# Optimization experiments

Hardware: AMD Instinct MI355X
Metric: run time of the kernel (lower is better)

The kernel has to match this reference:

```python
import math
import jax, jax.numpy as jnp
from jax import lax
import numpy as np

SCORE_THR = 0.5
IOU_THR = 0.7
MIN_SIZE = 1.0
BBOX_CLIP = math.log(1000.0 / 16.0)

FEAT_SIZES = [100, 50, 25, 13, 7]
STRIDES = [8, 16, 32, 64, 128]
RATIOS = (0.5, 1.0, 2.0)
C = 256
A = 3
N = 2


def _make_priors(fs, stride):
    base = stride * 4.0
    ys, xs = np.meshgrid(np.arange(fs), np.arange(fs), indexing='ij')
    cx = (xs + 0.5) * stride
    cy = (ys + 0.5) * stride
    pri = []
    for r in RATIOS:
        w = base / np.sqrt(r)
        h = base * np.sqrt(r)
        pri.append(np.stack([cx - w / 2, cy - h / 2, cx + w / 2, cy + h / 2], axis=-1))
    pri = np.stack(pri, axis=2)  # (fs, fs, A, 4): H,W,A order matches permute/reshape
    return jnp.asarray(pri.reshape(-1, 4), dtype=jnp.float32)


def setup_inputs():
    key = jax.random.key(0)
    ks = jax.random.split(key, 8)
    inp = {}
    for i, fs in enumerate(FEAT_SIZES):
        inp[f'fmap{i}'] = jax.random.normal(jax.random.fold_in(ks[0], i), (N, C, fs, fs), dtype=jnp.float32)
        inp[f'priors{i}'] = _make_priors(fs, STRIDES[i])
    sc = 0.02
    inp['conv_w'] = jax.random.normal(ks[1], (C, C, 3, 3), jnp.float32) * sc
    inp['conv_b'] = jnp.zeros((C,), jnp.float32)
    inp['log_w'] = jax.random.normal(ks[2], (A, C, 1, 1), jnp.float32) * sc
    inp['log_b'] = jnp.zeros((A,), jnp.float32)
    inp['reg_w'] = jax.random.normal(ks[3], (A * 4, C, 1, 1), jnp.float32) * sc
    inp['reg_b'] = jnp.zeros((A * 4,), jnp.float32)
    inp['imsizes'] = jnp.full((N, 2), 800, dtype=jnp.int32)  # (h, w) per image
    inp['lvtop'] = 500
    inp['imtop'] = 100
    return inp


def _conv(x, w, b, pad):
    y = lax.conv_general_dilated(x, w, (1, 1), pad, dimension_numbers=('NCHW', 'OIHW', 'NCHW'))
    return y + b[None, :, None, None]


def _decode(reg, pri):
    pw = pri[..., 2] - pri[..., 0]
    ph = pri[..., 3] - pri[..., 1]
    pcx = pri[..., 0] + 0.5 * pw
    pcy = pri[..., 1] + 0.5 * ph
    dx, dy = reg[..., 0], reg[..., 1]
    dw = jnp.minimum(reg[..., 2], BBOX_CLIP)
    dh = jnp.minimum(reg[..., 3], BBOX_CLIP)
    cx = dx * pw + pcx
    cy = dy * ph + pcy
    w = jnp.exp(dw) * pw
    h = jnp.exp(dh) * ph
    return jnp.stack([cx - 0.5 * w, cy - 0.5 * h, cx + 0.5 * w, cy + 0.5 * h], axis=-1)


def _head(x, priors, conv_w, conv_b, log_w, log_b, reg_w, reg_b, lvtop):
    n = x.shape[0]
    h = jax.nn.relu(_conv(x, conv_w, conv_b, 'SAME'))
    reg = _conv(h, reg_w, reg_b, 'VALID').transpose(0, 2, 3, 1).reshape(n, -1, 4)
    log = _conv(h, log_w, log_b, 'VALID').transpose(0, 2, 3, 1).reshape(n, -1)
    k = min(lvtop, log.shape[1])
    vals, top = lax.top_k(log, k)                           # (n, k)
    reg = jnp.take_along_axis(reg, top[..., None], axis=1)  # (n, k, 4)
    pri = priors[top]                                       # (n, k, 4)
    return _decode(reg, pri), vals, k


def _box_iou(a, b):
    area_a = (a[:, 2] - a[:, 0]) * (a[:, 3] - a[:, 1])
    area_b = (b[:, 2] - b[:, 0]) * (b[:, 3] - b[:, 1])
    lt = jnp.maximum(a[:, None, :2], b[None, :, :2])
    rb = jnp.minimum(a[:, None, 2:], b[None, :, 2:])
    wh = jnp.clip(rb - lt, 0.0)
    inter = wh[..., 0] * wh[..., 1]
    return inter / (area_a[:, None] + area_b[None, :] - inter + 1e-9)


def _forward(fmaps, priors, conv_w, conv_b, log_w, log_b, reg_w, reg_b, imsizes, lvtop, imtop):
    tups = [_head(x, p, conv_w, conv_b, log_w, log_b, reg_w, reg_b, lvtop)
            for x, p in zip(fmaps, priors)]
    boxes = jnp.concatenate([t[0] for t in tups], axis=1)                 # (n, D, 4)
    obj = jax.nn.sigmoid(jnp.concatenate([t[1] for t in tups], axis=1))   # (n, D)
    lvlen = jnp.asarray([t[2] for t in tups])
    n, D = obj.shape
    boxes = boxes.reshape(-1, 4)
    obj = obj.reshape(-1)
    K = n * D
    imidx = jnp.arange(K) // D
    valid = obj >= SCORE_THR                                # score filter (masked, not nonzero)
    hw = imsizes[imidx].astype(jnp.float32)                 # (K, 2) = (h, w)
    x1 = jnp.clip(boxes[:, 0], 0.0, hw[:, 1])
    y1 = jnp.clip(boxes[:, 1], 0.0, hw[:, 0])
    x2 = jnp.clip(boxes[:, 2], 0.0, hw[:, 1])
    y2 = jnp.clip(boxes[:, 3], 0.0, hw[:, 0])
    boxes = jnp.stack([x1, y1, x2, y2], axis=-1)
    valid &= (x2 - x1 >= MIN_SIZE) & (y2 - y1 >= MIN_SIZE)  # remove_small
    lvidx = jnp.searchsorted(jnp.cumsum(lvlen), jnp.arange(K) % D, side='right')
    groups = imidx * 10 + lvidx
    scores = jnp.where(valid, obj, -jnp.inf)
    order = jnp.argsort(-scores)                            # global score order; groups gate suppression
    b, g, v, ii = boxes[order], groups[order], valid[order], imidx[order]
    iou = _box_iou(b, b)                                    # (K, K)
    ar = jnp.arange(K)
    def body(i, keep):
        sup = (iou[i] > IOU_THR) & (g == g[i]) & (ar > i)
        return jnp.where(keep[i], keep & ~sup, keep)
    keep = lax.fori_loop(0, K, body, v)                     # greedy batched NMS
    def select(i):
        m = keep & (ii == i)
        sel = jnp.argsort(~m)[:imtop]                       # stable: kept boxes in score order
        val = m[sel]
        bx = jnp.where(val[:, None], b[sel], 0.0)
        ix = jnp.where(val, i, -1)
        return bx, ix
    bx, ix = jax.vmap(select)(jnp.arange(n))
    return bx.reshape(n * imtop, 4), ix.reshape(n * imtop)


def reference(fmap0, fmap1, fmap2, fmap3, fmap4, priors0, priors1, priors2, priors3, priors4,
              conv_w, conv_b, log_w, log_b, reg_w, reg_b, imsizes, lvtop, imtop):
    return _forward([fmap0, fmap1, fmap2, fmap3, fmap4],
                    [priors0, priors1, priors2, priors3, priors4],
                    conv_w, conv_b, log_w, log_b, reg_w, reg_b, imsizes, lvtop, imtop)
```

## Files before the change

kernel.cpp:

```cpp
#include <hip/hip_runtime.h>
#include <math.h>


#define N_IMG 2
#define C_CH  256
#define D_PER 2147
#define K_TOT 4294
#define CONV_BLOCKS 1912
#define CPX 239

typedef double v4d __attribute__((ext_vector_type(4)));

__constant__ int c_Ml[5]     = {30000, 7500, 1875, 507, 147};
__constant__ int c_kl[5]     = {500, 500, 500, 500, 147};
__constant__ int c_logoff[5] = {0, 60000, 75000, 78750, 79764};
__constant__ int c_regoff[5] = {0, 240000, 300000, 315000, 319056};
__constant__ int c_fs[5]     = {100, 50, 25, 13, 7};
__constant__ int c_npt[5]    = {13, 7, 4, 2, 1};
__constant__ int c_E[5]      = {10000, 2500, 625, 169, 49};
__constant__ int c_cumbl[6]  = {0, 1352, 1744, 1872, 1904, 1912};
__constant__ int c_hcum[6]   = {0, 157, 197, 207, 210, 211};
__constant__ size_t c_hoff[5] = {0, 5120000, 6400000, 6720000, 6806528};

template <typename T>
__global__ __launch_bounds__(256) void conv_fused_kernel(
    const float* __restrict__ x0, const float* __restrict__ x1,
    const float* __restrict__ x2, const float* __restrict__ x3,
    const float* __restrict__ x4, const float* __restrict__ wraw,
    const float* __restrict__ bias, T* __restrict__ h) {
  __shared__ __align__(16) double s_in[2][960];
  int tid = threadIdx.x;
  int bid = (blockIdx.x & 7) * CPX + (blockIdx.x >> 3);
  int l = 0;
  while (bid >= c_cumbl[l + 1]) ++l;
  int r = bid - c_cumbl[l];
  int fs = c_fs[l], npt = c_npt[l];
  int tiles = npt * npt;
  int tile = r % tiles;
  int cn = r / tiles;
  int cobi = cn & 3, n = cn >> 2;
  int ptx = tile % npt, pty = tile / npt;
  int px0 = ptx * 8, py0 = pty * 8;
  int E = fs * fs;
  const float* xl;
  switch (l) {
    case 0: xl = x0; break;
    case 1: xl = x1; break;
    case 2: xl = x2; break;
    case 3: xl = x3; break;
    default: xl = x4; break;
  }
  const float* xn = xl + (size_t)n * C_CH * E;
  T* hl = h + c_hoff[l];

  int lane = tid & 63;
  int wv = tid >> 6;
  int lx = lane & 15;
  int lk = lane >> 4;

  double ind0 = (lk == 0) ? 1.0 : 0.0;
  v4d pr1 = __builtin_amdgcn_mfma_f64_16x16x4f64((double)lx, ind0,
                                                 (v4d)0.0, 0, 0, 0);
  v4d pr2 = __builtin_amdgcn_mfma_f64_16x16x4f64(ind0, (double)lx,
                                                 (v4d)0.0, 0, 0, 0);
  int coL[4], pxL[4];
#pragma unroll
  for (int q = 0; q < 4; ++q) {
    coL[q] = (int)pr1[q];
    pxL[q] = (int)pr2[q];
  }

  int in_dst[4], in_src[4];
#pragma unroll
  for (int it = 0; it < 4; ++it) {
    int idx = tid + it * 256;
    in_dst[it] = -1;
    in_src[it] = -1;
    if (idx < 800) {
      int ci = idx / 100, rr2 = idx % 100;
      int hy = rr2 / 10, hx = rr2 % 10;
      int gy = py0 - 1 + hy, gx = px0 - 1 + hx;
      in_dst[it] = ci * 120 + hy * 12 + hx;
      if (gy >= 0 && gy < fs && gx >= 0 && gx < fs)
        in_src[it] = ci * E + gy * fs + gx;
    }
  }

  int bOff[4];
#pragma unroll
  for (int p = 0; p < 4; ++p) {
    int pxidx = p * 16 + lx;
    bOff[p] = lk * 120 + (pxidx >> 3) * 12 + (pxidx & 7);
  }

  v4d acc[4];
#pragma unroll
  for (int p = 0; p < 4; ++p) acc[p] = (v4d)0.0;

  const float* wp0 =
      wraw + (size_t)(cobi * 64 + wv * 16 + lx) * 2304;

  float wcur[18], wnxt[18];
  {
    const float* a = wp0 + lk * 9;
    const float* b = wp0 + (4 + lk) * 9;
#pragma unroll
    for (int t = 0; t < 9; ++t) {
      wcur[t] = a[t];
      wcur[9 + t] = b[t];
    }
  }
  {
    float v0[4];
#pragma unroll
    for (int it = 0; it < 4; ++it)
      v0[it] = (in_dst[it] >= 0 && in_src[it] >= 0) ? xn[in_src[it]] : 0.f;
#pragma unroll
    for (int it = 0; it < 4; ++it)
      if (in_dst[it] >= 0) s_in[0][in_dst[it]] = (double)v0[it];
  }
  __syncthreads();

  for (int it = 0; it < 32; ++it) {
    int buf = it & 1;
    bool more = (it + 1 < 32);
    float inx[4];
    if (more) {
      const float* xc1 = xn + (size_t)(it + 1) * 8 * E;
#pragma unroll
      for (int s = 0; s < 4; ++s)
        inx[s] = (in_dst[s] >= 0 && in_src[s] >= 0) ? xc1[in_src[s]] : 0.f;
      const float* a = wp0 + ((it + 1) * 8 + lk) * 9;
      const float* b = wp0 + ((it + 1) * 8 + 4 + lk) * 9;
#pragma unroll
      for (int t = 0; t < 9; ++t) {
        wnxt[t] = a[t];
        wnxt[9 + t] = b[t];
      }
    }
    const double* bbA = s_in[buf];
    const double* bbB = s_in[buf] + 480;
#pragma unroll
    for (int ky = 0; ky < 3; ++ky) {
#pragma unroll
      for (int kx = 0; kx < 3; ++kx) {
        int tap = ky * 3 + kx;
        int boff = ky * 12 + kx;
        double avA = (double)wcur[tap];
#pragma unroll
        for (int p = 0; p < 4; ++p) {
          acc[p] = __builtin_amdgcn_mfma_f64_16x16x4f64(
              avA, bbA[bOff[p] + boff], acc[p], 0, 0, 0);
        }
      }
    }
#pragma unroll
    for (int ky = 0; ky < 3; ++ky) {
#pragma unroll
      for (int kx = 0; kx < 3; ++kx) {
        int tap = ky * 3 + kx;
        int boff = ky * 12 + kx;
        double avB = (double)wcur[9 + tap];
#pragma unroll
        for (int p = 0; p < 4; ++p) {
          acc[p] = __builtin_amdgcn_mfma_f64_16x16x4f64(
              avB, bbB[bOff[p] + boff], acc[p], 0, 0, 0);
        }
      }
    }
    if (more) {
      double* db = s_in[buf ^ 1];
#pragma unroll
      for (int s = 0; s < 4; ++s)
        if (in_dst[s] >= 0) db[in_dst[s]] = (double)inx[s];
#pragma unroll
      for (int t = 0; t < 18; ++t) wcur[t] = wnxt[t];
    }
    __syncthreads();
  }

#pragma unroll
  for (int p = 0; p < 4; ++p) {
#pragma unroll
    for (int rr2 = 0; rr2 < 4; ++rr2) {
      int pxidx = p * 16 + pxL[rr2];
      int gy = py0 + (pxidx >> 3), gx = px0 + (pxidx & 7);
      int co = cobi * 64 + wv * 16 + coL[rr2];
      if (gy < fs && gx < fs) {
        double v = acc[p][rr2] + (double)bias[co];
        hl[((size_t)n * C_CH + co) * E + gy * fs + gx] = (T)fmax(v, 0.0);
      }
    }
  }
}

template <typename T>
__global__ __launch_bounds__(256) void heads_fused_kernel(
    const T* __restrict__ h, const float* __restrict__ logw,
    const float* __restrict__ logb, const float* __restrict__ regw,
    const float* __restrict__ regb, double* __restrict__ logits,
    double* __restrict__ regs) {
  __shared__ float s_wh[256][16];
  __shared__ double s_red[4][15][64];
  int tid = threadIdx.x;
  int n = blockIdx.y;
  int cidx = blockIdx.x;
  int l = 0;
  while (cidx >= c_hcum[l + 1]) ++l;
  int chunk = cidx - c_hcum[l];
  int E = c_E[l];
  int px0 = chunk * 64;
  const T* hl = h + c_hoff[l];
  double* logits_l = logits + c_logoff[l];
  double* regs_l = regs + c_regoff[l];

  for (int idx = tid; idx < 4096; idx += 256) {
    int c = idx >> 4, j = idx & 15;
    float v = 0.f;
    if (j < 3) v = logw[j * 256 + c];
    else if (j < 15) v = regw[(j - 3) * 256 + c];
    s_wh[c][j] = v;
  }
  __syncthreads();

  int p = tid & 63, c4 = tid >> 6;
  int pix = px0 + p;
  bool act = pix < E;
  double acc[15];
#pragma unroll
  for (int j = 0; j < 15; j++) acc[j] = 0.0;
  if (act) {
    const T* hp = hl + ((size_t)n * C_CH + c4 * 64) * E + pix;
    for (int cc = 0; cc < 64; ++cc) {
      double hv = (double)hp[(size_t)cc * E];
      const float* wr = &s_wh[c4 * 64 + cc][0];
#pragma unroll
      for (int j = 0; j < 15; j++)
        acc[j] = fma((double)wr[j], hv, acc[j]);
    }
  }
#pragma unroll
  for (int j = 0; j < 15; j++) s_red[c4][j][p] = acc[j];
  __syncthreads();
  if (act) {
    int M = E * 3;
    for (int j = c4; j < 15; j += 4) {
      double v = s_red[0][j][p] + s_red[1][j][p] + s_red[2][j][p] +
                 s_red[3][j][p];
      if (j < 3) {
        logits_l[(size_t)n * M + pix * 3 + j] = v + (double)logb[j];
      } else {
        int rj = j - 3, a = rj >> 2, coord = rj & 3;
        regs_l[((size_t)n * M + pix * 3 + a) * 4 + coord] =
            v + (double)regb[rj];
      }
    }
  }
}

__device__ __forceinline__ unsigned long long d2key(double v) {
  unsigned long long ub = (unsigned long long)__double_as_longlong(v);
  return (ub >> 63) ? ~ub : (ub | 0x8000000000000000ull);
}

#define TK_CH 30
union TkShared {
  struct {
    int histw[16][256];
    int hist[256];
    int sgt[1024];
    int seq[1024];
  } a;
  struct {
    unsigned long long u[512];
    int idx[512];
    int keep[512];
    int ps[512];
    int m;
    double bx[512][4];
    unsigned long long mask[512][8];
  } b;
};

__global__ __launch_bounds__(1024) void topk_nms_kernel(
    const double* __restrict__ logits, const double* __restrict__ regs,
    const float* __restrict__ p0, const float* __restrict__ p1,
    const float* __restrict__ p2, const float* __restrict__ p3,
    const float* __restrict__ p4, const int* __restrict__ imsizes,
    double* __restrict__ g_box, unsigned long long* __restrict__ g_u,
    int* __restrict__ g_cnt) {
  __shared__ TkShared sh;
  __shared__ int s_sel[512];
  __shared__ unsigned long long s_prefix;
  __shared__ int s_r;
  int bid = blockIdx.x;
  int n = bid / 5, l = bid % 5;
  int M = c_Ml[l], k = c_kl[l];
  const double* lg = logits + c_logoff[l] + (size_t)n * M;
  int tid = threadIdx.x;
  if (tid == 0) { s_prefix = 0ull; s_r = k; }

  int chunk = (M + 1023) >> 10;
  int i0 = tid * chunk, i1 = min(M, i0 + chunk);
  int cnt = i1 - i0;
  if (cnt < 0) cnt = 0;
  unsigned long long kv[TK_CH];
#pragma unroll
  for (int q = 0; q < TK_CH; q++)
    if (q < cnt) kv[q] = d2key(lg[i0 + q]);
  int wid = tid >> 6;
  __syncthreads();

  for (int pass = 0; pass < 8; ++pass) {
    int shift = 56 - pass * 8;
    for (int i = tid; i < 4096; i += 1024) ((int*)sh.a.histw)[i] = 0;
    __syncthreads();
    unsigned long long pfx = s_prefix;
    int rr = s_r;
#pragma unroll
    for (int q = 0; q < TK_CH; q++) {
      if (q < cnt) {
        unsigned long long u = kv[q];
        if (pass == 0 || (u >> (shift + 8)) == pfx)
          atomicAdd(&sh.a.histw[wid][(int)((u >> shift) & 255ull)], 1);
      }
    }
    __syncthreads();
    if (tid < 256) {
      int s = 0;
#pragma unroll
      for (int w = 0; w < 16; w++) s += sh.a.histw[w][tid];
      sh.a.hist[tid] = s;
    }
    __syncthreads();
    if (tid == 0) {
      int s = 0, beta = 0;
      for (int b = 255; b >= 0; --b) {
        if (s + sh.a.hist[b] >= rr) { beta = b; break; }
        s += sh.a.hist[b];
      }
      s_prefix = (pfx << 8) | (unsigned long long)beta;
      s_r = rr - s;
    }
    __syncthreads();
  }
  unsigned long long T = s_prefix;
  int need = s_r;
  int cgt = 0, ceq = 0;
#pragma unroll
  for (int q = 0; q < TK_CH; q++) {
    if (q < cnt) {
      cgt += (kv[q] > T);
      ceq += (kv[q] == T);
    }
  }
  sh.a.sgt[tid] = cgt;
  sh.a.seq[tid] = ceq;
  __syncthreads();
  for (int o = 1; o < 1024; o <<= 1) {
    int a = (tid >= o) ? sh.a.sgt[tid - o] : 0;
    int b2 = (tid >= o) ? sh.a.seq[tid - o] : 0;
    __syncthreads();
    sh.a.sgt[tid] += a;
    sh.a.seq[tid] += b2;
    __syncthreads();
  }
  int gt_total = sh.a.sgt[1023];
  int pg = sh.a.sgt[tid] - cgt, pe = sh.a.seq[tid] - ceq;
#pragma unroll
  for (int q = 0; q < TK_CH; q++) {
    if (q < cnt) {
      unsigned long long u = kv[q];
      if (u > T) {
        s_sel[pg++] = i0 + q;
      } else if (u == T) {
        if (pe < need) s_sel[gt_total + pe] = i0 + q;
        pe++;
      }
    }
  }
  __syncthreads();

  const float* pp;
  switch (l) {
    case 0: pp = p0; break;
    case 1: pp = p1; break;
    case 2: pp = p2; break;
    case 3: pp = p3; break;
    default: pp = p4; break;
  }
  const double* regs_l = regs + c_regoff[l];
  double imh = (double)imsizes[n * 2 + 0], imw = (double)imsizes[n * 2 + 1];
  const double BCLIP = 4.1351665567423560;
  if (tid < 512) {
    unsigned long long key = 0ull;
    sh.b.idx[tid] = tid;
    sh.b.keep[tid] = 0;
    if (tid < k) {
      int aidx = s_sel[tid];
      double lv = lg[aidx];
      double obj = 1.0 / (1.0 + exp(-lv));
      const double* rp = regs_l + ((size_t)n * M + aidx) * 4;
      const float* pr = pp + (size_t)aidx * 4;
      double px1 = pr[0], py1 = pr[1], px2 = pr[2], py2 = pr[3];
      double pw = px2 - px1, ph = py2 - py1;
      double pcx = px1 + 0.5 * pw, pcy = py1 + 0.5 * ph;
      double dx = rp[0], dy = rp[1];
      double dw = fmin(rp[2], BCLIP), dh = fmin(rp[3], BCLIP);
      double cx = dx * pw + pcx, cy = dy * ph + pcy;
      double w = exp(dw) * pw, hh = exp(dh) * ph;
      double x1 = cx - 0.5 * w, y1 = cy - 0.5 * hh;
      double x2 = cx + 0.5 * w, y2 = cy + 0.5 * hh;
      x1 = fmin(fmax(x1, 0.0), imw);
      x2 = fmin(fmax(x2, 0.0), imw);
      y1 = fmin(fmax(y1, 0.0), imh);
      y2 = fmin(fmax(y2, 0.0), imh);
      bool valid = (obj >= 0.5) && ((x2 - x1) >= 1.0) && ((y2 - y1) >= 1.0);
      sh.b.bx[tid][0] = x1;
      sh.b.bx[tid][1] = y1;
      sh.b.bx[tid][2] = x2;
      sh.b.bx[tid][3] = y2;
      if (valid) key = d2key(obj);
    }
    sh.b.u[tid] = key;
  }
  if (tid == 0) sh.b.m = 0;
  __syncthreads();

  for (int kk = 2; kk <= 512; kk <<= 1) {
    for (int j = kk >> 1; j > 0; j >>= 1) {
      if (tid < 512) {
        int i = tid, ixj = i ^ j;
        if (ixj > i) {
          unsigned long long ua = sh.b.u[i], ub = sh.b.u[ixj];
          int ia = sh.b.idx[i], ib = sh.b.idx[ixj];
          bool up = ((i & kk) == 0);
          bool aAfterB = (ua < ub) || (ua == ub && ia > ib);
          bool sw = up ? aAfterB : !aAfterB && (ua != ub || ia != ib);
          if (sw) {
            sh.b.u[i] = ub; sh.b.u[ixj] = ua;
            sh.b.idx[i] = ib; sh.b.idx[ixj] = ia;
          }
        }
      }
      __syncthreads();
    }
  }
  if (tid < 512) {
    if (sh.b.u[tid] != 0ull && (tid == 511 || sh.b.u[tid + 1] == 0ull))
      sh.b.m = tid + 1;
  }
  __syncthreads();
  int m = sh.b.m;

  if (tid < 512 && tid < m) {
    int i = tid;
    const double* A = sh.b.bx[sh.b.idx[i]];
    double ax1 = A[0], ay1 = A[1], ax2 = A[2], ay2 = A[3];
    double areaA = (ax2 - ax1) * (ay2 - ay1);
    unsigned long long row[8] = {0, 0, 0, 0, 0, 0, 0, 0};
    for (int j = i + 1; j < m; ++j) {
      const double* B = sh.b.bx[sh.b.idx[j]];
      double bx1 = B[0], by1 = B[1], bx2 = B[2], by2 = B[3];
      double areaB = (bx2 - bx1) * (by2 - by1);
      double lx = fmax(ax1, bx1), ly = fmax(ay1, by1);
      double rx = fmin(ax2, bx2), ry = fmin(ay2, by2);
      double iw = fmax(rx - lx, 0.0), ih = fmax(ry - ly, 0.0);
      double inter = iw * ih;
      double iou = inter / (areaA + areaB - inter + 1e-9);
      if (iou > 0.7) row[j >> 6] |= (1ull << (j & 63));
    }
#pragma unroll
    for (int w2 = 0; w2 < 8; ++w2) sh.b.mask[i][w2] = row[w2];
  }
  __syncthreads();

  if (tid == 0) {
    unsigned long long remv[8] = {0, 0, 0, 0, 0, 0, 0, 0};
    for (int i = 0; i < m; ++i) {
      if (!((remv[i >> 6] >> (i & 63)) & 1ull)) {
        sh.b.keep[i] = 1;
#pragma unroll
        for (int w2 = 0; w2 < 8; ++w2) remv[w2] |= sh.b.mask[i][w2];
      }
    }
  }
  __syncthreads();

  if (tid < 512) sh.b.ps[tid] = sh.b.keep[tid];
  __syncthreads();
  for (int o = 1; o < 512; o <<= 1) {
    int v = 0;
    if (tid < 512 && tid >= o) v = sh.b.ps[tid - o];
    __syncthreads();
    if (tid < 512) sh.b.ps[tid] += v;
    __syncthreads();
  }
  if (tid < 512 && sh.b.keep[tid]) {
    int pos = sh.b.ps[tid] - 1;
    const double* B = sh.b.bx[sh.b.idx[tid]];
    size_t gbase = (size_t)bid * 512 + pos;
#pragma unroll
    for (int q = 0; q < 4; q++) g_box[gbase * 4 + q] = B[q];
    g_u[gbase] = sh.b.u[tid];
  }
  if (tid == 0) g_cnt[bid] = (m > 0) ? sh.b.ps[511] : 0;
}

__global__ __launch_bounds__(256) void select_kernel(
    const double* __restrict__ g_box, const unsigned long long* __restrict__ g_u,
    const int* __restrict__ g_cnt, float* __restrict__ out) {
  __shared__ unsigned long long s_u[5][512];
  __shared__ int s_pick[100];
  __shared__ int s_total;
  int n = blockIdx.x;
  int tid = threadIdx.x;
  int cnts[5];
#pragma unroll
  for (int l = 0; l < 5; l++) cnts[l] = g_cnt[n * 5 + l];
  for (int idx = tid; idx < 5 * 512; idx += 256) {
    int l = idx >> 9, r = idx & 511;
    s_u[l][r] = (r < cnts[l]) ? g_u[(size_t)(n * 5 + l) * 512 + r] : 0ull;
  }
  __syncthreads();
  if (tid == 0) {
    int hd[5] = {0, 0, 0, 0, 0};
    int t = 0;
    while (t < 100) {
      int bl = -1;
      unsigned long long bu = 0ull;
      for (int l = 0; l < 5; l++) {
        if (hd[l] < cnts[l] && s_u[l][hd[l]] > bu) {
          bu = s_u[l][hd[l]];
          bl = l;
        }
      }
      if (bl < 0) break;
      s_pick[t++] = bl * 512 + hd[bl];
      hd[bl]++;
    }
    s_total = t;
  }
  __syncthreads();
  int total = s_total;
  for (int t = tid; t < 100; t += 256) {
    if (t < total) {
      int pk = s_pick[t];
      int l = pk >> 9, r = pk & 511;
      size_t gbase = (size_t)(n * 5 + l) * 512 + r;
#pragma unroll
      for (int q = 0; q < 4; q++)
        out[(n * 100 + t) * 4 + q] = (float)g_box[gbase * 4 + q];
      out[800 + n * 100 + t] = (float)n;
    } else {
#pragma unroll
      for (int q = 0; q < 4; q++) out[(n * 100 + t) * 4 + q] = 0.0f;
      out[800 + n * 100 + t] = -1.0f;
    }
  }
}

extern "C" void kernel_launch(void* const* d_in, const int* in_sizes, int n_in,
                              void* d_out, int out_size, void* d_ws,
                              size_t ws_size, hipStream_t stream) {
  (void)in_sizes; (void)n_in; (void)out_size;
  const float* fmap[5];
  const float* priors[5];
  for (int l = 0; l < 5; l++) {
    fmap[l] = (const float*)d_in[2 * l];
    priors[l] = (const float*)d_in[2 * l + 1];
  }
  const float* conv_w = (const float*)d_in[10];
  const float* conv_b = (const float*)d_in[11];
  const float* log_w = (const float*)d_in[12];
  const float* log_b = (const float*)d_in[13];
  const float* reg_w = (const float*)d_in[14];
  const float* reg_b = (const float*)d_in[15];
  const int* imsizes = (const int*)d_in[16];
  float* out = (float*)d_out;

  bool f64h = ws_size >= (size_t)60000000;

  char* base = (char*)d_ws;
  size_t off = 0;
  auto alloc = [&](size_t bytes) -> void* {
    off = (off + 255) & ~(size_t)255;
    void* p = base + off;
    off += bytes;
    return p;
  };
  void* hraw = alloc(6831616ull * (f64h ? 8 : 4));
  double* logits = (double*)alloc(80058ull * 8);
  double* regs = (double*)alloc(320232ull * 8);
  double* g_box = (double*)alloc(10ull * 512 * 4 * 8);
  unsigned long long* g_u = (unsigned long long*)alloc(10ull * 512 * 8);
  int* g_cnt = (int*)alloc(10 * 4);

  if (f64h) {
    conv_fused_kernel<double><<<CONV_BLOCKS, 256, 0, stream>>>(
        fmap[0], fmap[1], fmap[2], fmap[3], fmap[4], conv_w, conv_b,
        (double*)hraw);
    heads_fused_kernel<double><<<dim3(211, 2), 256, 0, stream>>>(
        (double*)hraw, log_w, log_b, reg_w, reg_b, logits, regs);
  } else {
    conv_fused_kernel<float><<<CONV_BLOCKS, 256, 0, stream>>>(
        fmap[0], fmap[1], fmap[2], fmap[3], fmap[4], conv_w, conv_b,
        (float*)hraw);
    heads_fused_kernel<float><<<dim3(211, 2), 256, 0, stream>>>(
        (float*)hraw, log_w, log_b, reg_w, reg_b, logits, regs);
  }
  topk_nms_kernel<<<10, 1024, 0, stream>>>(
      logits, regs, priors[0], priors[1], priors[2], priors[3], priors[4],
      imsizes, g_box, g_u, g_cnt);
  select_kernel<<<2, 256, 0, stream>>>(g_box, g_u, g_cnt, out);
}
```

Before: 1.002 ms.

## Fuse 1x1 head convolutions into 3x3 conv epilogue with per-channel-block partial sums

The separate heads kernel and the large intermediate feature-map buffer are removed. Each conv block stages its ReLU output tile in shared memory (sharing space with the input staging buffer through a union) and computes partial logits and regression sums over its 64 output channels. The four partial sums are added, with the biases, inside the top-k/NMS kernel. This saves one launch and the global write and re-read of a roughly 6.8M-element tensor. In exchange it adds shared-memory traffic and a serial head epilogue to every conv block, and the top-k pass now reads four partial arrays.

```diff
diff --git a/kernel.cpp b/kernel.cpp
--- a/kernel.cpp
+++ b/kernel.cpp
@@ -8,6 +8,8 @@
 #define K_TOT 4294
 #define CONV_BLOCKS 1912
 #define CPX 239
+#define PLOG_N 80058
+#define PREG_N 320232
 
 typedef double v4d __attribute__((ext_vector_type(4)));
 
@@ -19,16 +21,20 @@
 __constant__ int c_npt[5]    = {13, 7, 4, 2, 1};
 __constant__ int c_E[5]      = {10000, 2500, 625, 169, 49};
 __constant__ int c_cumbl[6]  = {0, 1352, 1744, 1872, 1904, 1912};
-__constant__ int c_hcum[6]   = {0, 157, 197, 207, 210, 211};
-__constant__ size_t c_hoff[5] = {0, 5120000, 6400000, 6720000, 6806528};
-
-template <typename T>
+
 __global__ __launch_bounds__(256) void conv_fused_kernel(
     const float* __restrict__ x0, const float* __restrict__ x1,
     const float* __restrict__ x2, const float* __restrict__ x3,
     const float* __restrict__ x4, const float* __restrict__ wraw,
-    const float* __restrict__ bias, T* __restrict__ h) {
-  __shared__ __align__(16) double s_in[2][960];
+    const float* __restrict__ bias, const float* __restrict__ logw,
+    const float* __restrict__ regw, double* __restrict__ plog,
+    double* __restrict__ preg) {
+  union ShmU {
+    double s_in[2][960];
+    double s_h[64][65];
+  };
+  __shared__ __align__(16) ShmU shm;
+  __shared__ float s_wh[15][64];
   int tid = threadIdx.x;
   int bid = (blockIdx.x & 7) * CPX + (blockIdx.x >> 3);
   int l = 0;
@@ -51,12 +57,17 @@
     default: xl = x4; break;
   }
   const float* xn = xl + (size_t)n * C_CH * E;
-  T* hl = h + c_hoff[l];
 
   int lane = tid & 63;
   int wv = tid >> 6;
   int lx = lane & 15;
   int lk = lane >> 4;
+
+  for (int idx = tid; idx < 960; idx += 256) {
+    int j = idx / 64, co = idx & 63;
+    s_wh[j][co] = (j < 3) ? logw[j * 256 + cobi * 64 + co]
+                          : regw[(j - 3) * 256 + cobi * 64 + co];
+  }
 
   double ind0 = (lk == 0) ? 1.0 : 0.0;
   v4d pr1 = __builtin_amdgcn_mfma_f64_16x16x4f64((double)lx, ind0,
@@ -97,8 +108,7 @@
 #pragma unroll
   for (int p = 0; p < 4; ++p) acc[p] = (v4d)0.0;
 
-  const float* wp0 =
-      wraw + (size_t)(cobi * 64 + wv * 16 + lx) * 2304;
+  const float* wp0 = wraw + (size_t)(cobi * 64 + wv * 16 + lx) * 2304;
 
   float wcur[18], wnxt[18];
   {
@@ -117,7 +127,7 @@
       v0[it] = (in_dst[it] >= 0 && in_src[it] >= 0) ? xn[in_src[it]] : 0.f;
 #pragma unroll
     for (int it = 0; it < 4; ++it)
-      if (in_dst[it] >= 0) s_in[0][in_dst[it]] = (double)v0[it];
+      if (in_dst[it] >= 0) shm.s_in[0][in_dst[it]] = (double)v0[it];
   }
   __syncthreads();
 
@@ -138,8 +148,8 @@
         wnxt[9 + t] = b[t];
       }
     }
-    const double* bbA = s_in[buf];
-    const double* bbB = s_in[buf] + 480;
+    const double* bbA = shm.s_in[buf];
+    const double* bbB = shm.s_in[buf] + 480;
 #pragma unroll
     for (int ky = 0; ky < 3; ++ky) {
 #pragma unroll
@@ -169,7 +179,7 @@
       }
     }
     if (more) {
-      double* db = s_in[buf ^ 1];
+      double* db = shm.s_in[buf ^ 1];
 #pragma unroll
       for (int s = 0; s < 4; ++s)
         if (in_dst[s] >= 0) db[in_dst[s]] = (double)inx[s];
@@ -184,75 +194,43 @@
 #pragma unroll
     for (int rr2 = 0; rr2 < 4; ++rr2) {
       int pxidx = p * 16 + pxL[rr2];
-      int gy = py0 + (pxidx >> 3), gx = px0 + (pxidx & 7);
-      int co = cobi * 64 + wv * 16 + coL[rr2];
-      if (gy < fs && gx < fs) {
-        double v = acc[p][rr2] + (double)bias[co];
-        hl[((size_t)n * C_CH + co) * E + gy * fs + gx] = (T)fmax(v, 0.0);
-      }
-    }
-  }
-}
-
-template <typename T>
-__global__ __launch_bounds__(256) void heads_fused_kernel(
-    const T* __restrict__ h, const float* __restrict__ logw,
-    const float* __restrict__ logb, const float* __restrict__ regw,
-    const float* __restrict__ regb, double* __restrict__ logits,
-    double* __restrict__ regs) {
-  __shared__ float s_wh[256][16];
-  __shared__ double s_red[4][15][64];
-  int tid = threadIdx.x;
-  int n = blockIdx.y;
-  int cidx = blockIdx.x;
-  int l = 0;
-  while (cidx >= c_hcum[l + 1]) ++l;
-  int chunk = cidx - c_hcum[l];
-  int E = c_E[l];
-  int px0 = chunk * 64;
-  const T* hl = h + c_hoff[l];
-  double* logits_l = logits + c_logoff[l];
-  double* regs_l = regs + c_regoff[l];
-
-  for (int idx = tid; idx < 4096; idx += 256) {
-    int c = idx >> 4, j = idx & 15;
-    float v = 0.f;
-    if (j < 3) v = logw[j * 256 + c];
-    else if (j < 15) v = regw[(j - 3) * 256 + c];
-    s_wh[c][j] = v;
-  }
-  __syncthreads();
-
-  int p = tid & 63, c4 = tid >> 6;
-  int pix = px0 + p;
-  bool act = pix < E;
-  double acc[15];
-#pragma unroll
-  for (int j = 0; j < 15; j++) acc[j] = 0.0;
-  if (act) {
-    const T* hp = hl + ((size_t)n * C_CH + c4 * 64) * E + pix;
-    for (int cc = 0; cc < 64; ++cc) {
-      double hv = (double)hp[(size_t)cc * E];
-      const float* wr = &s_wh[c4 * 64 + cc][0];
-#pragma unroll
-      for (int j = 0; j < 15; j++)
-        acc[j] = fma((double)wr[j], hv, acc[j]);
-    }
-  }
-#pragma unroll
-  for (int j = 0; j < 15; j++) s_red[c4][j][p] = acc[j];
-  __syncthreads();
-  if (act) {
-    int M = E * 3;
-    for (int j = c4; j < 15; j += 4) {
-      double v = s_red[0][j][p] + s_red[1][j][p] + s_red[2][j][p] +
-                 s_red[3][j][p];
-      if (j < 3) {
-        logits_l[(size_t)n * M + pix * 3 + j] = v + (double)logb[j];
-      } else {
-        int rj = j - 3, a = rj >> 2, coord = rj & 3;
-        regs_l[((size_t)n * M + pix * 3 + a) * 4 + coord] =
-            v + (double)regb[rj];
+      int co_l = wv * 16 + coL[rr2];
+      int co = cobi * 64 + co_l;
+      double v = acc[p][rr2] + (double)bias[co];
+      shm.s_h[co_l][pxidx] = fmax(v, 0.0);
+    }
+  }
+  __syncthreads();
+
+  {
+    int px = tid & 63;
+    int jg = tid >> 6;
+    int gy = py0 + (px >> 3), gx = px0 + (px & 7);
+    double hs[4] = {0.0, 0.0, 0.0, 0.0};
+    for (int co = 0; co < 64; ++co) {
+      double hv = shm.s_h[co][px];
+#pragma unroll
+      for (int js = 0; js < 4; ++js) {
+        int j = js * 4 + jg;
+        if (j < 15) hs[js] = fma((double)s_wh[j][co], hv, hs[js]);
+      }
+    }
+    if (gy < fs && gx < fs) {
+      int pix = gy * fs + gx;
+      int M = c_Ml[l];
+      size_t abase = (size_t)n * M + (size_t)pix * 3;
+#pragma unroll
+      for (int js = 0; js < 4; ++js) {
+        int j = js * 4 + jg;
+        if (j >= 15) continue;
+        double v = hs[js];
+        if (j < 3) {
+          plog[(size_t)cobi * PLOG_N + c_logoff[l] + abase + j] = v;
+        } else {
+          int rj = j - 3, a = rj >> 2, coord = rj & 3;
+          preg[(size_t)cobi * PREG_N + c_regoff[l] + (abase + a) * 4 +
+               coord] = v;
+        }
       }
     }
   }
@@ -283,7 +261,8 @@
 };
 
 __global__ __launch_bounds__(1024) void topk_nms_kernel(
-    const double* __restrict__ logits, const double* __restrict__ regs,
+    const double* __restrict__ plog, const double* __restrict__ preg,
+    const float* __restrict__ logb, const float* __restrict__ regb,
     const float* __restrict__ p0, const float* __restrict__ p1,
     const float* __restrict__ p2, const float* __restrict__ p3,
     const float* __restrict__ p4, const int* __restrict__ imsizes,
@@ -296,7 +275,7 @@
   int bid = blockIdx.x;
   int n = bid / 5, l = bid % 5;
   int M = c_Ml[l], k = c_kl[l];
-  const double* lg = logits + c_logoff[l] + (size_t)n * M;
+  const double* lgc = plog + c_logoff[l] + (size_t)n * M;
   int tid = threadIdx.x;
   if (tid == 0) { s_prefix = 0ull; s_r = k; }
 
@@ -307,7 +286,12 @@
   unsigned long long kv[TK_CH];
 #pragma unroll
   for (int q = 0; q < TK_CH; q++)
-    if (q < cnt) kv[q] = d2key(lg[i0 + q]);
+    if (q < cnt) {
+      int i = i0 + q;
+      double lv = (double)logb[i % 3] + lgc[i] + lgc[PLOG_N + i] +
+                  lgc[2 * PLOG_N + i] + lgc[3 * PLOG_N + i];
+      kv[q] = d2key(lv);
+    }
   int wid = tid >> 6;
   __syncthreads();
 
@@ -389,7 +373,7 @@
     case 3: pp = p3; break;
     default: pp = p4; break;
   }
-  const double* regs_l = regs + c_regoff[l];
+  const double* rgc = preg + c_regoff[l];
   double imh = (double)imsizes[n * 2 + 0], imw = (double)imsizes[n * 2 + 1];
   const double BCLIP = 4.1351665567423560;
   if (tid < 512) {
@@ -398,15 +382,24 @@
     sh.b.keep[tid] = 0;
     if (tid < k) {
       int aidx = s_sel[tid];
-      double lv = lg[aidx];
+      double lv = (double)logb[aidx % 3] + lgc[aidx] + lgc[PLOG_N + aidx] +
+                  lgc[2 * PLOG_N + aidx] + lgc[3 * PLOG_N + aidx];
       double obj = 1.0 / (1.0 + exp(-lv));
-      const double* rp = regs_l + ((size_t)n * M + aidx) * 4;
-      const float* pr = pp + (size_t)aidx * 4;
+      int a3 = aidx % 3;
+      size_t rb = ((size_t)n * M + aidx) * 4;
+      double rv[4];
+#pragma unroll
+      for (int coord = 0; coord < 4; ++coord)
+        rv[coord] = (double)regb[a3 * 4 + coord] + rgc[rb + coord] +
+                    rgc[PREG_N + rb + coord] + rgc[2 * PREG_N + rb + coord] +
+                    rgc[3 * PREG_N + rb + coord];
+      const float* pr = pp + (size_t)(aidx / 3) * 12 + (size_t)(aidx % 3) * 4;
+      pr = pp + (size_t)aidx * 4;
       double px1 = pr[0], py1 = pr[1], px2 = pr[2], py2 = pr[3];
       double pw = px2 - px1, ph = py2 - py1;
       double pcx = px1 + 0.5 * pw, pcy = py1 + 0.5 * ph;
-      double dx = rp[0], dy = rp[1];
-      double dw = fmin(rp[2], BCLIP), dh = fmin(rp[3], BCLIP);
+      double dx = rv[0], dy = rv[1];
+      double dw = fmin(rv[2], BCLIP), dh = fmin(rv[3], BCLIP);
       double cx = dx * pw + pcx, cy = dy * ph + pcy;
       double w = exp(dw) * pw, hh = exp(dh) * ph;
       double x1 = cx - 0.5 * w, y1 = cy - 0.5 * hh;
@@ -563,7 +556,7 @@
 extern "C" void kernel_launch(void* const* d_in, const int* in_sizes, int n_in,
                               void* d_out, int out_size, void* d_ws,
                               size_t ws_size, hipStream_t stream) {
-  (void)in_sizes; (void)n_in; (void)out_size;
+  (void)in_sizes; (void)n_in; (void)out_size; (void)ws_size;
   const float* fmap[5];
   const float* priors[5];
   for (int l = 0; l < 5; l++) {
@@ -579,8 +572,6 @@
   const int* imsizes = (const int*)d_in[16];
   float* out = (float*)d_out;
 
-  bool f64h = ws_size >= (size_t)60000000;
-
   char* base = (char*)d_ws;
   size_t off = 0;
   auto alloc = [&](size_t bytes) -> void* {
@@ -589,28 +580,17 @@
     off += bytes;
     return p;
   };
-  void* hraw = alloc(6831616ull * (f64h ? 8 : 4));
-  double* logits = (double*)alloc(80058ull * 8);
-  double* regs = (double*)alloc(320232ull * 8);
+  double* plog = (double*)alloc(4ull * PLOG_N * 8);
+  double* preg = (double*)alloc(4ull * PREG_N * 8);
   double* g_box = (double*)alloc(10ull * 512 * 4 * 8);
   unsigned long long* g_u = (unsigned long long*)alloc(10ull * 512 * 8);
   int* g_cnt = (int*)alloc(10 * 4);
 
-  if (f64h) {
-    conv_fused_kernel<double><<<CONV_BLOCKS, 256, 0, stream>>>(
-        fmap[0], fmap[1], fmap[2], fmap[3], fmap[4], conv_w, conv_b,
-        (double*)hraw);
-    heads_fused_kernel<double><<<dim3(211, 2), 256, 0, stream>>>(
-        (double*)hraw, log_w, log_b, reg_w, reg_b, logits, regs);
-  } else {
-    conv_fused_kernel<float><<<CONV_BLOCKS, 256, 0, stream>>>(
-        fmap[0], fmap[1], fmap[2], fmap[3], fmap[4], conv_w, conv_b,
-        (float*)hraw);
-    heads_fused_kernel<float><<<dim3(211, 2), 256, 0, stream>>>(
-        (float*)hraw, log_w, log_b, reg_w, reg_b, logits, regs);
-  }
+  conv_fused_kernel<<<CONV_BLOCKS, 256, 0, stream>>>(
+      fmap[0], fmap[1], fmap[2], fmap[3], fmap[4], conv_w, conv_b, log_w,
+      reg_w, plog, preg);
   topk_nms_kernel<<<10, 1024, 0, stream>>>(
-      logits, regs, priors[0], priors[1], priors[2], priors[3], priors[4],
-      imsizes, g_box, g_u, g_cnt);
+      plog, preg, log_b, reg_b, priors[0], priors[1], priors[2], priors[3],
+      priors[4], imsizes, g_box, g_u, g_cnt);
   select_kernel<<<2, 256, 0, stream>>>(g_box, g_u, g_cnt, out);
 }
```

New measurement: 1.068 ms. +6.5%, slower.

## Fuse final select into topk kernel via last-block atomic counter, simplify tie handling

Applied to the files above, without the earlier changes.

Removes the separate select kernel launch. The last topk block to finish, found with a global atomic counter that the conv kernel resets, now runs the cross-level merge and writes the output. It also switches the logits load to a strided (coalesced) pattern and replaces the second prefix scan for ties with an atomic append plus a single-thread insertion sort, capped at 128 ties. This saves one launch and a scan, at the cost of a serialized tail in one block and a cap on the tie count.

```diff
diff --git a/kernel.cpp b/kernel.cpp
--- a/kernel.cpp
+++ b/kernel.cpp
@@ -27,9 +27,11 @@
     const float* __restrict__ x0, const float* __restrict__ x1,
     const float* __restrict__ x2, const float* __restrict__ x3,
     const float* __restrict__ x4, const float* __restrict__ wraw,
-    const float* __restrict__ bias, T* __restrict__ h) {
+    const float* __restrict__ bias, T* __restrict__ h,
+    int* __restrict__ g_sync) {
   __shared__ __align__(16) double s_in[2][960];
   int tid = threadIdx.x;
+  if (blockIdx.x == 0 && tid == 0) *g_sync = 0;
   int bid = (blockIdx.x & 7) * CPX + (blockIdx.x >> 3);
   int l = 0;
   while (bid >= c_cumbl[l + 1]) ++l;
@@ -97,8 +99,7 @@
 #pragma unroll
   for (int p = 0; p < 4; ++p) acc[p] = (v4d)0.0;
 
-  const float* wp0 =
-      wraw + (size_t)(cobi * 64 + wv * 16 + lx) * 2304;
+  const float* wp0 = wraw + (size_t)(cobi * 64 + wv * 16 + lx) * 2304;
 
   float wcur[18], wnxt[18];
   {
@@ -269,7 +270,6 @@
     int histw[16][256];
     int hist[256];
     int sgt[1024];
-    int seq[1024];
   } a;
   struct {
     unsigned long long u[512];
@@ -280,6 +280,11 @@
     double bx[512][4];
     unsigned long long mask[512][8];
   } b;
+  struct {
+    unsigned long long su[5][512];
+    int pick[100];
+    int total;
+  } c;
 };
 
 __global__ __launch_bounds__(1024) void topk_nms_kernel(
@@ -288,26 +293,29 @@
     const float* __restrict__ p2, const float* __restrict__ p3,
     const float* __restrict__ p4, const int* __restrict__ imsizes,
     double* __restrict__ g_box, unsigned long long* __restrict__ g_u,
-    int* __restrict__ g_cnt) {
+    int* __restrict__ g_cnt, int* __restrict__ g_sync,
+    float* __restrict__ out) {
   __shared__ TkShared sh;
   __shared__ int s_sel[512];
+  __shared__ int s_tie[128];
+  __shared__ int s_tienum;
   __shared__ unsigned long long s_prefix;
   __shared__ int s_r;
+  __shared__ int s_rank;
   int bid = blockIdx.x;
   int n = bid / 5, l = bid % 5;
   int M = c_Ml[l], k = c_kl[l];
   const double* lg = logits + c_logoff[l] + (size_t)n * M;
   int tid = threadIdx.x;
-  if (tid == 0) { s_prefix = 0ull; s_r = k; }
-
-  int chunk = (M + 1023) >> 10;
-  int i0 = tid * chunk, i1 = min(M, i0 + chunk);
-  int cnt = i1 - i0;
+  if (tid == 0) { s_prefix = 0ull; s_r = k; s_tienum = 0; }
+
+  int cnt = (M - tid + 1023) >> 10;
   if (cnt < 0) cnt = 0;
+  if (cnt > TK_CH) cnt = TK_CH;
   unsigned long long kv[TK_CH];
 #pragma unroll
   for (int q = 0; q < TK_CH; q++)
-    if (q < cnt) kv[q] = d2key(lg[i0 + q]);
+    if (q < cnt) kv[q] = d2key(lg[tid + (q << 10)]);
   int wid = tid >> 6;
   __syncthreads();
 
@@ -346,38 +354,44 @@
   }
   unsigned long long T = s_prefix;
   int need = s_r;
-  int cgt = 0, ceq = 0;
-#pragma unroll
-  for (int q = 0; q < TK_CH; q++) {
-    if (q < cnt) {
-      cgt += (kv[q] > T);
-      ceq += (kv[q] == T);
-    }
-  }
+  int cgt = 0;
+#pragma unroll
+  for (int q = 0; q < TK_CH; q++)
+    if (q < cnt) cgt += (kv[q] > T);
   sh.a.sgt[tid] = cgt;
-  sh.a.seq[tid] = ceq;
   __syncthreads();
   for (int o = 1; o < 1024; o <<= 1) {
     int a = (tid >= o) ? sh.a.sgt[tid - o] : 0;
-    int b2 = (tid >= o) ? sh.a.seq[tid - o] : 0;
     __syncthreads();
     sh.a.sgt[tid] += a;
-    sh.a.seq[tid] += b2;
     __syncthreads();
   }
   int gt_total = sh.a.sgt[1023];
-  int pg = sh.a.sgt[tid] - cgt, pe = sh.a.seq[tid] - ceq;
+  int pg = sh.a.sgt[tid] - cgt;
 #pragma unroll
   for (int q = 0; q < TK_CH; q++) {
     if (q < cnt) {
       unsigned long long u = kv[q];
+      int i = tid + (q << 10);
       if (u > T) {
-        s_sel[pg++] = i0 + q;
+        s_sel[pg++] = i;
       } else if (u == T) {
-        if (pe < need) s_sel[gt_total + pe] = i0 + q;
-        pe++;
-      }
-    }
+        int pos = atomicAdd(&s_tienum, 1);
+        if (pos < 128) s_tie[pos] = i;
+      }
+    }
+  }
+  __syncthreads();
+  if (tid == 0) {
+    int tn = s_tienum;
+    if (tn > 128) tn = 128;
+    for (int a = 1; a < tn; ++a) {
+      int v = s_tie[a], b = a - 1;
+      while (b >= 0 && s_tie[b] > v) { s_tie[b + 1] = s_tie[b]; --b; }
+      s_tie[b + 1] = v;
+    }
+    if (need > tn) need = tn;
+    for (int r2 = 0; r2 < need; ++r2) s_sel[gt_total + r2] = s_tie[r2];
   }
   __syncthreads();
 
@@ -505,58 +519,59 @@
     g_u[gbase] = sh.b.u[tid];
   }
   if (tid == 0) g_cnt[bid] = (m > 0) ? sh.b.ps[511] : 0;
-}
-
-__global__ __launch_bounds__(256) void select_kernel(
-    const double* __restrict__ g_box, const unsigned long long* __restrict__ g_u,
-    const int* __restrict__ g_cnt, float* __restrict__ out) {
-  __shared__ unsigned long long s_u[5][512];
-  __shared__ int s_pick[100];
-  __shared__ int s_total;
-  int n = blockIdx.x;
-  int tid = threadIdx.x;
-  int cnts[5];
-#pragma unroll
-  for (int l = 0; l < 5; l++) cnts[l] = g_cnt[n * 5 + l];
-  for (int idx = tid; idx < 5 * 512; idx += 256) {
-    int l = idx >> 9, r = idx & 511;
-    s_u[l][r] = (r < cnts[l]) ? g_u[(size_t)(n * 5 + l) * 512 + r] : 0ull;
-  }
-  __syncthreads();
-  if (tid == 0) {
-    int hd[5] = {0, 0, 0, 0, 0};
-    int t = 0;
-    while (t < 100) {
-      int bl = -1;
-      unsigned long long bu = 0ull;
-      for (int l = 0; l < 5; l++) {
-        if (hd[l] < cnts[l] && s_u[l][hd[l]] > bu) {
-          bu = s_u[l][hd[l]];
-          bl = l;
+  __syncthreads();
+
+  __threadfence();
+  if (tid == 0) s_rank = atomicAdd(g_sync, 1);
+  __syncthreads();
+  if (s_rank != 9) return;
+
+  for (int nn = 0; nn < N_IMG; ++nn) {
+    int cnts[5];
+#pragma unroll
+    for (int l2 = 0; l2 < 5; l2++) cnts[l2] = g_cnt[nn * 5 + l2];
+    for (int idx = tid; idx < 5 * 512; idx += 1024) {
+      int l2 = idx >> 9, r2 = idx & 511;
+      sh.c.su[l2][r2] =
+          (r2 < cnts[l2]) ? g_u[(size_t)(nn * 5 + l2) * 512 + r2] : 0ull;
+    }
+    __syncthreads();
+    if (tid == 0) {
+      int hd[5] = {0, 0, 0, 0, 0};
+      int t = 0;
+      while (t < 100) {
+        int bl = -1;
+        unsigned long long bu = 0ull;
+        for (int l2 = 0; l2 < 5; l2++) {
+          if (hd[l2] < cnts[l2] && sh.c.su[l2][hd[l2]] > bu) {
+            bu = sh.c.su[l2][hd[l2]];
+            bl = l2;
+          }
         }
-      }
-      if (bl < 0) break;
-      s_pick[t++] = bl * 512 + hd[bl];
-      hd[bl]++;
-    }
-    s_total = t;
-  }
-  __syncthreads();
-  int total = s_total;
-  for (int t = tid; t < 100; t += 256) {
-    if (t < total) {
-      int pk = s_pick[t];
-      int l = pk >> 9, r = pk & 511;
-      size_t gbase = (size_t)(n * 5 + l) * 512 + r;
-#pragma unroll
-      for (int q = 0; q < 4; q++)
-        out[(n * 100 + t) * 4 + q] = (float)g_box[gbase * 4 + q];
-      out[800 + n * 100 + t] = (float)n;
-    } else {
-#pragma unroll
-      for (int q = 0; q < 4; q++) out[(n * 100 + t) * 4 + q] = 0.0f;
-      out[800 + n * 100 + t] = -1.0f;
-    }
+        if (bl < 0) break;
+        sh.c.pick[t++] = bl * 512 + hd[bl];
+        hd[bl]++;
+      }
+      sh.c.total = t;
+    }
+    __syncthreads();
+    int total = sh.c.total;
+    for (int t = tid; t < 100; t += 1024) {
+      if (t < total) {
+        int pk = sh.c.pick[t];
+        int l2 = pk >> 9, r2 = pk & 511;
+        size_t gbase = (size_t)(nn * 5 + l2) * 512 + r2;
+#pragma unroll
+        for (int q = 0; q < 4; q++)
+          out[(nn * 100 + t) * 4 + q] = (float)g_box[gbase * 4 + q];
+        out[800 + nn * 100 + t] = (float)nn;
+      } else {
+#pragma unroll
+        for (int q = 0; q < 4; q++) out[(nn * 100 + t) * 4 + q] = 0.0f;
+        out[800 + nn * 100 + t] = -1.0f;
+      }
+    }
+    __syncthreads();
   }
 }
 
@@ -594,23 +609,23 @@
   double* regs = (double*)alloc(320232ull * 8);
   double* g_box = (double*)alloc(10ull * 512 * 4 * 8);
   unsigned long long* g_u = (unsigned long long*)alloc(10ull * 512 * 8);
-  int* g_cnt = (int*)alloc(10 * 4);
+  int* g_cnt = (int*)alloc(16 * 4);
+  int* g_sync = (int*)alloc(4);
 
   if (f64h) {
     conv_fused_kernel<double><<<CONV_BLOCKS, 256, 0, stream>>>(
         fmap[0], fmap[1], fmap[2], fmap[3], fmap[4], conv_w, conv_b,
-        (double*)hraw);
+        (double*)hraw, g_sync);
     heads_fused_kernel<double><<<dim3(211, 2), 256, 0, stream>>>(
         (double*)hraw, log_w, log_b, reg_w, reg_b, logits, regs);
   } else {
     conv_fused_kernel<float><<<CONV_BLOCKS, 256, 0, stream>>>(
         fmap[0], fmap[1], fmap[2], fmap[3], fmap[4], conv_w, conv_b,
-        (float*)hraw);
+        (float*)hraw, g_sync);
     heads_fused_kernel<float><<<dim3(211, 2), 256, 0, stream>>>(
         (float*)hraw, log_w, log_b, reg_w, reg_b, logits, regs);
   }
   topk_nms_kernel<<<10, 1024, 0, stream>>>(
       logits, regs, priors[0], priors[1], priors[2], priors[3], priors[4],
-      imsizes, g_box, g_u, g_cnt);
-  select_kernel<<<2, 256, 0, stream>>>(g_box, g_u, g_cnt, out);
+      imsizes, g_box, g_u, g_cnt, g_sync, out);
 }
```

New measurement: 1.038 ms. 1.04x slower.
